# Optimization experiments

Measured on AMD Instinct MI355X. Metric: run time of the kernel, lower is better.

The kernel has to match this reference:

```python
import jax, jax.numpy as jnp
import numpy as np

B, S, D = 2, 2048, 2048
NH = 16
HD = D // NH  # 128
MAX_POS = 4096
ROPE_THETA = 10000.0


def rotate_half(x):
    x1, x2 = x[..., : x.shape[-1] // 2], x[..., x.shape[-1] // 2 :]
    return jnp.concatenate((-x2, x1), axis=-1)


def rope_tables(dtype=jnp.float32):
    inv_freq = 1.0 / (ROPE_THETA ** (jnp.arange(0, HD, 2, dtype=jnp.float32) / HD))
    t = jnp.arange(MAX_POS, dtype=jnp.float32)
    freqs = jnp.outer(t, inv_freq)              # [MAX_POS, HD/2]
    emb = jnp.concatenate((freqs, freqs), axis=-1)  # [MAX_POS, HD]
    return jnp.cos(emb).astype(dtype), jnp.sin(emb).astype(dtype)


def setup_inputs() -> dict:
    key = jax.random.key(0)
    ks = jax.random.split(key, 9)
    sc = 0.02
    return {
        "hidden_states": jax.random.normal(ks[0], (B, S, D), jnp.float32),
        "position_ids": jnp.arange(B * S, dtype=jnp.int32).reshape(B, S),
        "Wq": jax.random.normal(ks[1], (D, D), jnp.float32) * sc,
        "bq": jax.random.normal(ks[2], (D,), jnp.float32) * sc,
        "Wk": jax.random.normal(ks[3], (D, D), jnp.float32) * sc,
        "bk": jax.random.normal(ks[4], (D,), jnp.float32) * sc,
        "Wv": jax.random.normal(ks[5], (D, D), jnp.float32) * sc,
        "bv": jax.random.normal(ks[6], (D,), jnp.float32) * sc,
        "Wo": jax.random.normal(ks[7], (D, D), jnp.float32) * sc,
    }


def reference(hidden_states, position_ids, Wq, bq, Wk, bk, Wv, bv, Wo):
    b, s, _ = hidden_states.shape
    # projections (torch Linear: x @ W.T + b)
    q = (hidden_states @ Wq.T + bq).reshape(b, s, NH, HD).transpose(0, 2, 1, 3)
    k = (hidden_states @ Wk.T + bk).reshape(b, s, NH, HD).transpose(0, 2, 1, 3)
    v = (hidden_states @ Wv.T + bv).reshape(b, s, NH, HD).transpose(0, 2, 1, 3)
    # RoPE
    cos_t, sin_t = rope_tables(hidden_states.dtype)
    cos = cos_t[position_ids][:, None, :, :]  # [B,1,S,HD]
    sin = sin_t[position_ids][:, None, :, :]
    q = q * cos + rotate_half(q) * sin
    k = k * cos + rotate_half(k) * sin
    # NOTE: faithful to the source bug — softmax is computed but its result is
    # discarded; the AV matmul uses the UNNORMALIZED scaled scores.
    attn_weights = jnp.einsum("bhqd,bhkd->bhqk", q, k) / (HD ** 0.5)
    _ = jax.nn.softmax(attn_weights.astype(jnp.float32), axis=-1)  # dead, as in source
    attn_output = jnp.einsum("bhqk,bhkd->bhqd", attn_weights, v)
    attn_output = attn_output.transpose(0, 2, 1, 3).reshape(b, s, D)
    return attn_output @ Wo.T
```

## Files before the change

### kernel.cpp

```cpp
#include <hip/hip_runtime.h>
#include <hip/hip_bf16.h>


typedef __attribute__((ext_vector_type(8))) short bf16x8s;
typedef __attribute__((ext_vector_type(4))) float f32x4;

__device__ __forceinline__ ushort f2bf(float f) {
    union { float f; unsigned int u; } x; x.f = f;
    unsigned int u = x.u;
    unsigned int r = (u + 0x7fffu + ((u >> 16) & 1u)) >> 16;
    return (ushort)r;
}
__device__ __forceinline__ float b2f(ushort u) {
    union { unsigned int u; float f; } x; x.u = ((unsigned int)u) << 16;
    return x.f;
}

__device__ __forceinline__ void gload_lds16(const void* g, void* l) {
    __builtin_amdgcn_global_load_lds((__attribute__((address_space(1))) const void*)g,
                                     (__attribute__((address_space(3))) void*)l, 16, 0, 0);
}

template<bool BIAS, bool OBF16, int BN>
__global__ __launch_bounds__(256)
void gemm_nt(const ushort* __restrict__ A, const ushort* __restrict__ B,
             const float* __restrict__ bias, void* __restrict__ Cv,
             int K, int lda, int ldb, int ldc, int ZH,
             long sAb, long sAh, long sBb, long sBh, long sCb, long sCh)
{
    __shared__ ushort As[128 * 32];
    __shared__ ushort Bs[BN * 32];

    int z  = blockIdx.z;
    int zb = z / ZH, zh = z - zb * ZH;
    const ushort* Ab = A + (size_t)(sAb * zb + sAh * zh);
    const ushort* Bb = B + (size_t)(sBb * zb + sBh * zh);
    size_t Coff = (size_t)(sCb * zb + sCh * zh);

    int m0 = blockIdx.x * 128, n0 = blockIdx.y * BN;
    int t = threadIdx.x;
    int l = t & 63, w = t >> 6;
    int wm, wn;
    if (BN == 128) { wm = (w >> 1) * 64; wn = (w & 1) * 64; }
    else           { wm = w * 32;        wn = 0; }
    constexpr int FM = (BN == 128) ? 4 : 2;
    constexpr int FN = 4;
    int lr = l & 15, lk = (l >> 4) * 8;

    f32x4 acc[FM][FN];
#pragma unroll
    for (int i = 0; i < FM; i++)
#pragma unroll
        for (int j = 0; j < FN; j++)
            acc[i][j] = (f32x4){0.f, 0.f, 0.f, 0.f};

    int c0 = t, c1 = t + 256;
    int r0 = c0 >> 2, k0c = (c0 & 3) * 8;
    int r1 = c1 >> 2, k1c = (c1 & 3) * 8;

    for (int kt = 0; kt < K; kt += 32) {
        __syncthreads();
        gload_lds16(Ab + (size_t)(m0 + r0) * lda + kt + k0c, &As[c0 * 8]);
        gload_lds16(Ab + (size_t)(m0 + r1) * lda + kt + k1c, &As[c1 * 8]);
        gload_lds16(Bb + (size_t)(n0 + r0) * ldb + kt + k0c, &Bs[c0 * 8]);
        if (BN == 128)
            gload_lds16(Bb + (size_t)(n0 + r1) * ldb + kt + k1c, &Bs[c1 * 8]);
        __syncthreads();

        bf16x8s af[FM], bf[FN];
#pragma unroll
        for (int i = 0; i < FM; i++)
            af[i] = *(const bf16x8s*)&As[(wm + i * 16 + lr) * 32 + lk];
#pragma unroll
        for (int i = 0; i < FN; i++)
            bf[i] = *(const bf16x8s*)&Bs[(wn + i * 16 + lr) * 32 + lk];
#pragma unroll
        for (int mi = 0; mi < FM; mi++)
#pragma unroll
            for (int ni = 0; ni < FN; ni++)
                acc[mi][ni] = __builtin_amdgcn_mfma_f32_16x16x32_bf16(
                    af[mi], bf[ni], acc[mi][ni], 0, 0, 0);
    }

    int rr = (l >> 4) * 4;
#pragma unroll
    for (int mi = 0; mi < FM; mi++) {
#pragma unroll
        for (int ni = 0; ni < FN; ni++) {
            int gr = m0 + wm + mi * 16 + rr;
            int gc = n0 + wn + ni * 16 + lr;
            float bv = BIAS ? bias[gc] : 0.f;
#pragma unroll
            for (int r = 0; r < 4; r++) {
                float v = acc[mi][ni][r] + bv;
                size_t off = Coff + (size_t)(gr + r) * ldc + gc;
                if (OBF16) ((ushort*)Cv)[off] = f2bf(v);
                else       ((float*)Cv)[off]  = v;
            }
        }
    }
}

__global__ __launch_bounds__(256)
void rope_qk(ushort* __restrict__ QKV, const int* __restrict__ pos,
             ushort* __restrict__ QB)
{
    int tid = blockIdx.x * 256 + threadIdx.x;
    int row = tid >> 7;
    int r = tid & 127;
    int h = r >> 3, j = r & 7;
    int d0 = j * 8;
    float p = (float)pos[row];
    size_t qb = (size_t)row * 6144 + h * 128 + d0;

    bf16x8s q1 = *(const bf16x8s*)&QKV[qb];
    bf16x8s q2 = *(const bf16x8s*)&QKV[qb + 64];
    bf16x8s k1 = *(const bf16x8s*)&QKV[qb + 2048];
    bf16x8s k2 = *(const bf16x8s*)&QKV[qb + 2048 + 64];
    bf16x8s oq1, oq2, ok1, ok2;
#pragma unroll
    for (int i = 0; i < 8; i++) {
        float d = (float)(d0 + i);
        float ang = p * exp2f(d * (-13.287712379549449f / 64.0f));
        float s, c;
        sincosf(ang, &s, &c);
        float a = b2f((ushort)q1[i]), b = b2f((ushort)q2[i]);
        oq1[i] = (short)f2bf(a * c - b * s);
        oq2[i] = (short)f2bf(b * c + a * s);
        float e = b2f((ushort)k1[i]), f = b2f((ushort)k2[i]);
        ok1[i] = (short)f2bf(e * c - f * s);
        ok2[i] = (short)f2bf(f * c + e * s);
    }
    size_t ob = (size_t)row * 2048 + h * 128 + d0;
    *(bf16x8s*)&QB[ob]      = oq1;
    *(bf16x8s*)&QB[ob + 64] = oq2;
    *(bf16x8s*)&QKV[qb + 2048]      = ok1;
    *(bf16x8s*)&QKV[qb + 2048 + 64] = ok2;
}

__global__ __launch_bounds__(256)
void ktv_partial(const ushort* __restrict__ QKV, float* __restrict__ part)
{
    int bh = blockIdx.x;
    int b = bh >> 4, h = bh & 15;
    int s0 = blockIdx.y * 128;
    const ushort* Kp = QKV + (size_t)(b * 2048 + s0) * 6144 + 2048 + h * 128;
    const ushort* Vp = Kp + 2048;

    __shared__ ushort Ks[32][128];
    __shared__ ushort Vs[32][128];

    int t = threadIdx.x;
    int tx = t & 15, ty = t >> 4;
    float acc[8][8];
#pragma unroll
    for (int i = 0; i < 8; i++)
#pragma unroll
        for (int j = 0; j < 8; j++) acc[i][j] = 0.f;

    for (int sb = 0; sb < 128; sb += 32) {
        __syncthreads();
#pragma unroll
        for (int i = 0; i < 2; i++) {
            int idx = t + i * 256;
            int rw = idx >> 4, c8 = (idx & 15) * 8;
            *(bf16x8s*)&Ks[rw][c8] = *(const bf16x8s*)&Kp[(size_t)(sb + rw) * 6144 + c8];
            *(bf16x8s*)&Vs[rw][c8] = *(const bf16x8s*)&Vp[(size_t)(sb + rw) * 6144 + c8];
        }
        __syncthreads();
        for (int ss = 0; ss < 32; ss++) {
            bf16x8s kvv = *(const bf16x8s*)&Ks[ss][tx * 8];
            bf16x8s vvv = *(const bf16x8s*)&Vs[ss][ty * 8];
            float kv[8], vv[8];
#pragma unroll
            for (int i = 0; i < 8; i++) { kv[i] = b2f((ushort)kvv[i]); vv[i] = b2f((ushort)vvv[i]); }
#pragma unroll
            for (int i = 0; i < 8; i++)
#pragma unroll
                for (int j = 0; j < 8; j++)
                    acc[i][j] += kv[i] * vv[j];
        }
    }
    float* pp = part + ((size_t)blockIdx.y * 32 + bh) * 16384;
#pragma unroll
    for (int i = 0; i < 8; i++)
#pragma unroll
        for (int j = 0; j < 8; j++)
            pp[(tx * 8 + i) * 128 + (ty * 8 + j)] = acc[i][j];
}

__global__ __launch_bounds__(256)
void reduce_ktv(const float* __restrict__ part, ushort* __restrict__ Mb)
{
    int i = blockIdx.x * 256 + threadIdx.x;
    float s = 0.f;
#pragma unroll
    for (int p = 0; p < 16; p++) s += part[(size_t)p * 524288 + i];
    Mb[i] = f2bf(s * 0.08838834764831845f);
}

__global__ __launch_bounds__(256)
void conv_f32_bf16(const float* __restrict__ in, ushort* __restrict__ out, int n4)
{
    int i = blockIdx.x * 256 + threadIdx.x;
    if (i >= n4) return;
    float4 v = ((const float4*)in)[i];
    ushort4 o;
    o.x = f2bf(v.x); o.y = f2bf(v.y); o.z = f2bf(v.z); o.w = f2bf(v.w);
    ((ushort4*)out)[i] = o;
}

__global__ __launch_bounds__(256)
void conv_weights(const float* __restrict__ w0, const float* __restrict__ w1,
                  const float* __restrict__ w2, const float* __restrict__ w3,
                  ushort* __restrict__ qkv, ushort* __restrict__ wo)
{
    int i = blockIdx.x * 256 + threadIdx.x;
    int id = i >> 20;
    int off = i & 1048575;
    const float* src = (id == 0) ? w0 : (id == 1) ? w1 : (id == 2) ? w2 : w3;
    float4 v = ((const float4*)src)[off];
    ushort4 o;
    o.x = f2bf(v.x); o.y = f2bf(v.y); o.z = f2bf(v.z); o.w = f2bf(v.w);
    if (id < 3) ((ushort4*)qkv)[(size_t)id * 1048576 + off] = o;
    else        ((ushort4*)wo)[off] = o;
}

__global__ __launch_bounds__(256)
void pack_bias(const float* __restrict__ bq, const float* __restrict__ bk,
               const float* __restrict__ bv, float* __restrict__ bqkv)
{
    int i = blockIdx.x * 256 + threadIdx.x;
    float v = (i < 2048) ? bq[i] : (i < 4096) ? bk[i - 2048] : bv[i - 4096];
    bqkv[i] = v;
}

extern "C" void kernel_launch(void* const* d_in, const int* in_sizes, int n_in,
                              void* d_out, int out_size, void* d_ws, size_t ws_size,
                              hipStream_t stream)
{
    const float* hs = (const float*)d_in[0];
    const int*  pos = (const int*)d_in[1];
    const float* Wq = (const float*)d_in[2];
    const float* bq = (const float*)d_in[3];
    const float* Wk = (const float*)d_in[4];
    const float* bk = (const float*)d_in[5];
    const float* Wv = (const float*)d_in[6];
    const float* bv = (const float*)d_in[7];
    const float* Wo = (const float*)d_in[8];
    float* out = (float*)d_out;
    char* ws = (char*)d_ws;

    ushort* HSB  = (ushort*)(ws + 0);
    ushort* QB   = (ushort*)(ws + 0);
    ushort* WQKV = (ushort*)(ws + 16777216);
    ushort* NT   = (ushort*)(ws + 16777216);
    ushort* WOB  = (ushort*)(ws + 41943040);
    float*  BQKV = (float*)(ws + 50331648);
    ushort* QKVB = (ushort*)(ws + 50356224);
    ushort* MB   = (ushort*)(ws + 100687872);
    float*  PART = out;

    dim3 blk(256);

    conv_f32_bf16<<<8192, blk, 0, stream>>>(hs, HSB, 2097152);
    conv_weights<<<16384, blk, 0, stream>>>(Wq, Wk, Wv, Wo, WQKV, WOB);
    pack_bias<<<24, blk, 0, stream>>>(bq, bk, bv, BQKV);

    gemm_nt<true, true, 128><<<dim3(32, 48, 1), blk, 0, stream>>>(
        HSB, WQKV, BQKV, QKVB, 2048, 2048, 2048, 6144, 1, 0, 0, 0, 0, 0, 0);

    rope_qk<<<2048, blk, 0, stream>>>(QKVB, pos, QB);

    ktv_partial<<<dim3(32, 16, 1), blk, 0, stream>>>(QKVB, PART);
    reduce_ktv<<<2048, blk, 0, stream>>>(PART, MB);

    gemm_nt<false, true, 128><<<dim3(16, 1, 32), blk, 0, stream>>>(
        WOB, MB, nullptr, NT, 128, 2048, 128, 2048, 16,
        0, 128, 262144, 16384, 4194304, 128);

    gemm_nt<false, false, 64><<<dim3(16, 32, 2), blk, 0, stream>>>(
        QB, NT, nullptr, out, 2048, 2048, 2048, 2048, 1,
        4194304, 0, 4194304, 0, 4194304, 0);
}
```

Before: 408.8 us.

## Add 256x256-tile GEMM kernel with 4-stage LDS pipeline for QKV and output GEMMs

Introduces a new 512-thread GEMM kernel with 256x256 output tiles, XOR-swizzled LDS layout, direct global-to-LDS loads through a 4-buffer ring with two tiles in flight, and workgroup index swizzling. It replaces the 128-wide tile GEMM for the fused QKV projection and for the final output GEMM. Larger tiles raise arithmetic intensity and cut global traffic. The cost is 128KB of LDS per block, heavy register use, and fewer blocks (384 and 128), which may underfill the 256 CUs on the final GEMM.

```diff
diff --git a/kernel.cpp b/kernel.cpp
--- a/kernel.cpp
+++ b/kernel.cpp
@@ -19,6 +19,128 @@
 __device__ __forceinline__ void gload_lds16(const void* g, void* l) {
     __builtin_amdgcn_global_load_lds((__attribute__((address_space(1))) const void*)g,
                                      (__attribute__((address_space(3))) void*)l, 16, 0, 0);
+}
+
+template<bool BIAS, bool OBF16>
+__global__ __launch_bounds__(512, 2)
+void gemm256(const ushort* __restrict__ A, const ushort* __restrict__ B,
+             const float* __restrict__ bias, void* __restrict__ Cv,
+             int K, int lda, int ldb, int ldc,
+             long sAb, long sBb, long sCb)
+{
+    __shared__ char smem[131072];
+    char* ldsA = smem;
+    char* ldsB = smem + 65536;
+
+    int z = blockIdx.z;
+    const ushort* Ab = A + (size_t)sAb * z;
+    const ushort* Bb = B + (size_t)sBb * z;
+    size_t Coff = (size_t)sCb * z;
+
+    int nwgx = gridDim.x;
+    int nwg = nwgx * gridDim.y;
+    int wg = blockIdx.y * nwgx + blockIdx.x;
+    int swz = ((nwg & 7) == 0) ? (wg & 7) * (nwg >> 3) + (wg >> 3) : wg;
+    int m0 = (swz % nwgx) * 256;
+    int n0 = (swz / nwgx) * 256;
+
+    int tid = threadIdx.x;
+    int l = tid & 63, wid = tid >> 6;
+    int wm = (wid >> 2) * 128;
+    int wn = (wid & 3) * 64;
+    int lr = l & 15, lj = l >> 4;
+
+    int offA[8], offB[4];
+#pragma unroll
+    for (int m = 0; m < 8; m++) {
+        int r = wm + m * 16 + lr;
+        offA[m] = (r >> 1) * 128 + (((((r & 1) << 2) | lj) ^ ((r >> 1) & 7)) << 4);
+    }
+#pragma unroll
+    for (int n = 0; n < 4; n++) {
+        int r = wn + n * 16 + lr;
+        offB[n] = (r >> 1) * 128 + (((((r & 1) << 2) | lj) ^ ((r >> 1) & 7)) << 4);
+    }
+
+    size_t srcA[2], srcB[2];
+    int dstOff[2];
+#pragma unroll
+    for (int s = 0; s < 2; s++) {
+        int c = tid + s * 512;
+        int pr = c >> 3;
+        int up = (c & 7) ^ (pr & 7);
+        int r = (pr << 1) | (up >> 2);
+        int jj = up & 3;
+        srcA[s] = (size_t)(m0 + r) * lda + jj * 8;
+        srcB[s] = (size_t)(n0 + r) * ldb + jj * 8;
+        dstOff[s] = c * 16;
+    }
+
+    f32x4 acc[8][4];
+#pragma unroll
+    for (int m = 0; m < 8; m++)
+#pragma unroll
+        for (int n = 0; n < 4; n++)
+            acc[m][n] = (f32x4){0.f, 0.f, 0.f, 0.f};
+
+    int NT2 = K >> 5;
+
+#define STAGE256(T) { int _bo = ((T) & 3) * 16384; size_t _ko = (size_t)(T) * 32; \
+    gload_lds16(Ab + srcA[0] + _ko, ldsA + _bo + dstOff[0]); \
+    gload_lds16(Ab + srcA[1] + _ko, ldsA + _bo + dstOff[1]); \
+    gload_lds16(Bb + srcB[0] + _ko, ldsB + _bo + dstOff[0]); \
+    gload_lds16(Bb + srcB[1] + _ko, ldsB + _bo + dstOff[1]); }
+
+    STAGE256(0);
+    STAGE256(1);
+    asm volatile("s_waitcnt vmcnt(4)" ::: "memory");
+    __builtin_amdgcn_s_barrier();
+
+    for (int t = 0; t < NT2; ++t) {
+        if (t + 2 < NT2) {
+            STAGE256(t + 2);
+            __builtin_amdgcn_sched_barrier(0);
+        }
+        int bo = (t & 3) * 16384;
+        bf16x8s bf[4];
+#pragma unroll
+        for (int n = 0; n < 4; n++)
+            bf[n] = *(const bf16x8s*)(ldsB + bo + offB[n]);
+        bf16x8s af[8];
+#pragma unroll
+        for (int m = 0; m < 8; m++)
+            af[m] = *(const bf16x8s*)(ldsA + bo + offA[m]);
+#pragma unroll
+        for (int m = 0; m < 8; m++)
+#pragma unroll
+            for (int n = 0; n < 4; n++)
+                acc[m][n] = __builtin_amdgcn_mfma_f32_16x16x32_bf16(
+                    af[m], bf[n], acc[m][n], 0, 0, 0);
+        if (t + 1 < NT2) {
+            if (t + 2 < NT2) asm volatile("s_waitcnt vmcnt(4)" ::: "memory");
+            else             asm volatile("s_waitcnt vmcnt(0)" ::: "memory");
+            __builtin_amdgcn_s_barrier();
+        }
+    }
+#undef STAGE256
+
+    int rr = lj * 4;
+#pragma unroll
+    for (int m = 0; m < 8; m++) {
+#pragma unroll
+        for (int n = 0; n < 4; n++) {
+            int gr = m0 + wm + m * 16 + rr;
+            int gc = n0 + wn + n * 16 + lr;
+            float bv = BIAS ? bias[gc] : 0.f;
+#pragma unroll
+            for (int r = 0; r < 4; r++) {
+                float v = acc[m][n][r] + bv;
+                size_t off = Coff + (size_t)(gr + r) * ldc + gc;
+                if (OBF16) ((ushort*)Cv)[off] = f2bf(v);
+                else       ((float*)Cv)[off]  = v;
+            }
+        }
+    }
 }
 
 template<bool BIAS, bool OBF16, int BN>
@@ -267,8 +389,8 @@
     conv_weights<<<16384, blk, 0, stream>>>(Wq, Wk, Wv, Wo, WQKV, WOB);
     pack_bias<<<24, blk, 0, stream>>>(bq, bk, bv, BQKV);
 
-    gemm_nt<true, true, 128><<<dim3(32, 48, 1), blk, 0, stream>>>(
-        HSB, WQKV, BQKV, QKVB, 2048, 2048, 2048, 6144, 1, 0, 0, 0, 0, 0, 0);
+    gemm256<true, true><<<dim3(16, 24, 1), dim3(512), 0, stream>>>(
+        HSB, WQKV, BQKV, QKVB, 2048, 2048, 2048, 6144, 0, 0, 0);
 
     rope_qk<<<2048, blk, 0, stream>>>(QKVB, pos, QB);
 
@@ -279,7 +401,7 @@
         WOB, MB, nullptr, NT, 128, 2048, 128, 2048, 16,
         0, 128, 262144, 16384, 4194304, 128);
 
-    gemm_nt<false, false, 64><<<dim3(16, 32, 2), blk, 0, stream>>>(
-        QB, NT, nullptr, out, 2048, 2048, 2048, 2048, 1,
-        4194304, 0, 4194304, 0, 4194304, 0);
-}
+    gemm256<false, false><<<dim3(8, 8, 2), dim3(512), 0, stream>>>(
+        QB, NT, nullptr, out, 2048, 2048, 2048, 2048,
+        4194304, 4194304, 4194304);
+}
```

Result: faster. 393.2 us (-3.8%).
